# Kernel tuning notes

Hardware: AMD Instinct MI355X
Metric: run time of the kernel (lower is better)

Reference implementation:

```python
import math
import jax, jax.numpy as jnp
import numpy as np

H = 4  # num heads
D = 512
MLP = 1024
EPS = 1e-6


def _ln(x, g, b):
    m = x.mean(-1, keepdims=True)
    v = ((x - m) ** 2).mean(-1, keepdims=True)
    return (x - m) / jnp.sqrt(v + EPS) * g + b


def _heads(x):
    B, S, d = x.shape
    return x.reshape(B, S, H, d // H).transpose(0, 2, 1, 3)  # [B,H,S,hd]


def _att(q, k, v, Wo, bo):
    # q,k,v: [B,S,D] already projected
    hd = q.shape[-1] // H
    qh, kh, vh = _heads(q), _heads(k), _heads(v)
    scores = jnp.einsum('bhqd,bhkd->bhqk', qh, kh) / math.sqrt(hd)
    probs = jax.nn.softmax(scores, axis=-1)
    ctx = jnp.einsum('bhqk,bhkd->bhqd', probs, vh)
    B, _, S, _ = ctx.shape
    ctx = ctx.transpose(0, 2, 1, 3).reshape(B, S, H * hd)
    return ctx @ Wo + bo


def setup_inputs() -> dict:
    key = jax.random.key(0)
    ks = jax.random.split(key, 32)
    i = iter(range(32))
    def w(shape, scale=0.02):
        return jax.random.normal(ks[next(i)], shape, dtype=jnp.float32) * scale
    inp = {
        'x1': jax.random.normal(ks[next(i)], (16, 1024, D), dtype=jnp.float32),
        'x2': jax.random.normal(ks[next(i)], (16, 1024, D), dtype=jnp.float32),
        'ln1_g': jnp.ones((D,), jnp.float32), 'ln1_b': jnp.zeros((D,), jnp.float32),
        'ln2_g': jnp.ones((D,), jnp.float32), 'ln2_b': jnp.zeros((D,), jnp.float32),
        'lnf_g': jnp.ones((D,), jnp.float32), 'lnf_b': jnp.zeros((D,), jnp.float32),
    }
    for name in ['q1', 'k1', 'v1', 'q2', 'k2', 'v2', 'q12', 'k12', 'v12', 'o']:
        inp['W' + name] = w((D, D))
        inp['b' + name] = jnp.zeros((D,), jnp.float32)
    inp['W1'] = w((D, MLP)); inp['b1'] = jnp.zeros((MLP,), jnp.float32)
    inp['W2'] = w((MLP, D)); inp['b2'] = jnp.zeros((D,), jnp.float32)
    return inp


def reference(x1, x2, ln1_g, ln1_b, ln2_g, ln2_b, lnf_g, lnf_b,
              Wq1, bq1, Wk1, bk1, Wv1, bv1,
              Wq2, bq2, Wk2, bk2, Wv2, bv2,
              Wq12, bq12, Wk12, bk12, Wv12, bv12,
              Wo, bo, W1, b1, W2, b2):
    identity = x1
    x1n = _ln(x1, ln1_g, ln1_b)
    x2n = _ln(x2, ln2_g, ln2_b)
    # stream-1 self-attention with residual onto normalized input
    src1 = x1n + _att(x1n @ Wq1 + bq1, x1n @ Wk1 + bk1, x1n @ Wv1 + bv1, Wo, bo)
    # stream-2 self-attention
    src2 = x2n + _att(x2n @ Wq2 + bq2, x2n @ Wk2 + bk2, x2n @ Wv2 + bv2, Wo, bo)
    # cross attention: query from src1, key/value from src2
    attn_out = _att(src1 @ Wq12 + bq12, src2 @ Wk12 + bk12, src2 @ Wv12 + bv12, Wo, bo)
    x = attn_out + identity
    h = _ln(x, lnf_g, lnf_b)
    h = jax.nn.gelu(h @ W1 + b1, approximate=False) @ W2 + b2
    return x + h
```

## Files before the change

kernel.cpp:

```cpp
#include <hip/hip_runtime.h>
#include <math.h>


#define SEQ   1024
#define DM    512
#define HDIM  128
#define MTOK  16384
#define MLPD  1024
#define SC2   ((float)(0.08838834764831845 * 1.4426950408889634))

typedef short bf16x8 __attribute__((ext_vector_type(8)));
typedef float f32x4  __attribute__((ext_vector_type(4)));
typedef float f32x16 __attribute__((ext_vector_type(16)));
typedef unsigned short us4 __attribute__((ext_vector_type(4)));

typedef unsigned int u32g __attribute__((address_space(1)));
typedef unsigned int u32l __attribute__((address_space(3)));

static __device__ __forceinline__ unsigned short f2b(float f) {
  union { float f; unsigned u; } v; v.f = f;
  unsigned r = v.u + 0x7FFFu + ((v.u >> 16) & 1u);
  return (unsigned short)(r >> 16);
}
static __device__ __forceinline__ float b2f(unsigned short h) {
  union { unsigned u; float f; } v; v.u = ((unsigned)h) << 16;
  return v.f;
}
static __device__ __forceinline__ unsigned pk2t(float a, float b) {
  union { float f; unsigned u; } va, vb; va.f = a; vb.f = b;
  return __builtin_amdgcn_perm(vb.u, va.u, 0x07060302u);
}
static __device__ __forceinline__ void gl_lds16(const void* g, void* l) {
  __builtin_amdgcn_global_load_lds((u32g*)g, (u32l*)l, 16, 0, 0);
}

struct P12 { const float* p[12]; };
struct P9  { const float* p[9]; };

__global__ __launch_bounds__(256) void prep_kernel(P12 ws, P9 bs,
                                                   unsigned short* __restrict__ WT0,
                                                   unsigned short* __restrict__ W1t,
                                                   unsigned short* __restrict__ W2t,
                                                   float* __restrict__ bcc) {
  int bid = blockIdx.x;
  if (bid >= 3584) {
    int i = (bid - 3584) * 256 + threadIdx.x;
    if (i < 4608) bcc[i] = bs.p[i >> 9][i & 511];
    return;
  }
  __shared__ float t[32][33];
  const float* W; unsigned short* Wt; int K, N, tt;
  if (bid < 2560)      { int wi = bid >> 8; W = ws.p[wi]; Wt = WT0 + (size_t)wi * 262144; K = 512; N = 512; tt = bid & 255; }
  else if (bid < 3072) { W = ws.p[10]; Wt = W1t; K = 512;  N = 1024; tt = bid - 2560; }
  else                 { W = ws.p[11]; Wt = W2t; K = 1024; N = 512;  tt = bid - 3072; }
  int ntiles = N >> 5;
  int bx = tt % ntiles, by = tt / ntiles;
  int n0 = bx * 32, k0 = by * 32;
  int tx = threadIdx.x & 31, ty = threadIdx.x >> 5;
#pragma unroll
  for (int i = 0; i < 32; i += 8)
    t[ty + i][tx] = W[(size_t)(k0 + ty + i) * N + n0 + tx];
  __syncthreads();
#pragma unroll
  for (int i = 0; i < 32; i += 8)
    Wt[(size_t)(n0 + ty + i) * K + k0 + tx] = f2b(t[tx][ty + i]);
}

__global__ __launch_bounds__(256) void ln_kernel(const float* __restrict__ X0,
                                                 const float* __restrict__ X1,
                                                 const float* __restrict__ g0w,
                                                 const float* __restrict__ b0w,
                                                 const float* __restrict__ g1w,
                                                 const float* __restrict__ b1w,
                                                 unsigned short* __restrict__ out0,
                                                 unsigned short* __restrict__ out1) {
  int idx  = blockIdx.x * 4 + (threadIdx.x >> 6);
  int sel  = idx >> 14;
  int row  = idx & 16383;
  const float* X = sel ? X1 : X0;
  const float* gw = sel ? g1w : g0w;
  const float* bw = sel ? b1w : b0w;
  unsigned short* outB = sel ? out1 : out0;
  int lane = threadIdx.x & 63;
  const float4* xr = (const float4*)(X + (size_t)row * DM);
  float4 a = xr[lane];
  float4 c = xr[lane + 64];
  float s  = a.x + a.y + a.z + a.w + c.x + c.y + c.z + c.w;
  float s2 = a.x*a.x + a.y*a.y + a.z*a.z + a.w*a.w
           + c.x*c.x + c.y*c.y + c.z*c.z + c.w*c.w;
#pragma unroll
  for (int off = 1; off < 64; off <<= 1) {
    s  += __shfl_xor(s,  off, 64);
    s2 += __shfl_xor(s2, off, 64);
  }
  float mean = s * (1.0f / 512.0f);
  float var  = s2 * (1.0f / 512.0f) - mean * mean;
  float rstd = rsqrtf(var + 1e-6f);
  const float4* gv = (const float4*)gw;
  const float4* bv = (const float4*)bw;
  float4 g1 = gv[lane], g2 = gv[lane + 64];
  float4 b1 = bv[lane], b2 = bv[lane + 64];
  us4 o1, o2;
  o1.x = f2b((a.x - mean) * rstd * g1.x + b1.x);
  o1.y = f2b((a.y - mean) * rstd * g1.y + b1.y);
  o1.z = f2b((a.z - mean) * rstd * g1.z + b1.z);
  o1.w = f2b((a.w - mean) * rstd * g1.w + b1.w);
  o2.x = f2b((c.x - mean) * rstd * g2.x + b2.x);
  o2.y = f2b((c.y - mean) * rstd * g2.y + b2.y);
  o2.z = f2b((c.z - mean) * rstd * g2.z + b2.z);
  o2.w = f2b((c.w - mean) * rstd * g2.w + b2.w);
  *(us4*)(outB + (size_t)row * DM + lane * 4)        = o1;
  *(us4*)(outB + (size_t)row * DM + (lane + 64) * 4) = o2;
}

template <int RES, bool GELU_ACT, int OMODE>
__global__ __launch_bounds__(256) void gemm_kernel(const unsigned short* __restrict__ A,
                                                   const unsigned short* __restrict__ A1,
                                                   const unsigned short* __restrict__ Bt,
                                                   const float* __restrict__ bias,
                                                   const void* __restrict__ res,
                                                   float* __restrict__ outF,
                                                   unsigned short* __restrict__ outB,
                                                   unsigned short* __restrict__ outV,
                                                   int M, int N, int K) {
  int nT = N >> 7;
  int mT = M >> 7;
  int xcd = blockIdx.x & 7;
  int idx = blockIdx.x >> 3;
  int mPerX = mT >> 3;
  int q = idx / nT;
  int tm = xcd * mPerX + q;
  int tn = idx - q * nT;
  int m0 = tm << 7, n0 = tn << 7;
  int tid = threadIdx.x, lane = tid & 63, w = tid >> 6;
  int m16 = lane & 15, q4 = lane >> 4;
  int wr = (w & 1) << 6, wc = (w >> 1) << 6;
  __shared__ unsigned short Alds[128 * 64];
  __shared__ unsigned short Blds[128 * 64];
  f32x4 acc[4][4] = {};

  const unsigned short* Aeff = A;
  const unsigned short* Bteff = Bt;
  const float* biaseff = bias;
  if (OMODE == 3) {
    int half = tm >> 7;
    Bteff = Bt + (size_t)half * 3 * 262144;
    biaseff = bias + half * 1536;
  }
  if (OMODE == 4) {
    if (tn >= 4) Aeff = A1;
  }

  for (int k0 = 0; k0 < K; k0 += 64) {
    __syncthreads();
#pragma unroll
    for (int it = 0; it < 4; ++it) {
      int wf   = it * 2048 + w * 512;
      int flat = wf + lane * 8;
      int row  = flat >> 6, kk = flat & 63;
      gl_lds16(Aeff  + (size_t)(m0 + row) * K + k0 + kk, Alds + wf);
      gl_lds16(Bteff + (size_t)(n0 + row) * K + k0 + kk, Blds + wf);
    }
    __syncthreads();
#pragma unroll
    for (int kk = 0; kk < 64; kk += 32) {
      bf16x8 af[4], bfr[4];
#pragma unroll
      for (int i = 0; i < 4; ++i)
        af[i] = *(const bf16x8*)(Alds + (wr + i * 16 + m16) * 64 + kk + q4 * 8);
#pragma unroll
      for (int j = 0; j < 4; ++j)
        bfr[j] = *(const bf16x8*)(Blds + (wc + j * 16 + m16) * 64 + kk + q4 * 8);
#pragma unroll
      for (int i = 0; i < 4; ++i)
#pragma unroll
        for (int j = 0; j < 4; ++j)
          acc[i][j] = __builtin_amdgcn_mfma_f32_16x16x32_bf16(af[i], bfr[j], acc[i][j], 0, 0, 0);
    }
  }
  if (OMODE == 3 || OMODE == 4) {
    if (n0 < 1024) {
      int stride = (OMODE == 3) ? 1024 : 512;
      unsigned short* ob = outB;
      int coff = 0;
      if (OMODE == 4 && n0 >= 512) { ob = outB + (size_t)MTOK * 512; coff = 512; }
      float sc = (n0 < 512) ? SC2 : 1.0f;
#pragma unroll
      for (int i = 0; i < 4; ++i) {
#pragma unroll
        for (int r = 0; r < 4; ++r) {
          int row = m0 + wr + i * 16 + q4 * 4 + r;
#pragma unroll
          for (int j = 0; j < 4; ++j) {
            int col = n0 + wc + j * 16 + m16;
            ob[(size_t)row * stride + col - coff] = f2b((acc[i][j][r] + biaseff[col]) * sc);
          }
        }
      }
    } else {
#pragma unroll
      for (int i = 0; i < 4; ++i) {
        int row0 = m0 + wr + i * 16 + q4 * 4;
        int s = row0 & 1023, bl = row0 >> 10;
        s = (s & ~12) | ((s & 4) << 1) | ((s & 8) >> 1);
#pragma unroll
        for (int j = 0; j < 4; ++j) {
          int col = n0 + wc + j * 16 + m16;
          int hh = (col - 1024) >> 7, hd = col & 127;
          float bb = biaseff[col];
          us4 pkv;
          pkv.x = f2b(acc[i][j][0] + bb);
          pkv.y = f2b(acc[i][j][1] + bb);
          pkv.z = f2b(acc[i][j][2] + bb);
          pkv.w = f2b(acc[i][j][3] + bb);
          *(us4*)(outV + (((size_t)(bl * 4 + hh)) * HDIM + hd) * SEQ + s) = pkv;
        }
      }
    }
  } else {
#pragma unroll
    for (int i = 0; i < 4; ++i) {
#pragma unroll
      for (int r = 0; r < 4; ++r) {
        int row = m0 + wr + i * 16 + q4 * 4 + r;
#pragma unroll
        for (int j = 0; j < 4; ++j) {
          int col = n0 + wc + j * 16 + m16;
          float v = acc[i][j][r] + bias[col];
          if (RES == 1) v += ((const float*)res)[(size_t)row * N + col];
          if (RES == 2) v += b2f(((const unsigned short*)res)[(size_t)row * N + col]);
          if (GELU_ACT) v = 0.5f * v * (1.0f + erff(v * 0.70710678118654752f));
          if (OMODE == 1) outF[(size_t)row * N + col] = v;
          else            outB[(size_t)row * N + col] = f2b(v);
        }
      }
    }
  }
}

__global__ __launch_bounds__(256, 2) void attn_kernel(const unsigned short* __restrict__ Qb_,
                                                      const unsigned short* __restrict__ Kb_,
                                                      int tstride,
                                                      const unsigned short* __restrict__ Vt,
                                                      unsigned short* __restrict__ CTX,
                                                      int pairs_per_xcd) {
  int xcd = blockIdx.x & 7;
  int i   = blockIdx.x >> 3;
  int pair = xcd * pairs_per_xcd + (i >> 3);
  int qt   = i & 7;
  int b = pair >> 2, h = pair & 3;
  int tid = threadIdx.x, lane = tid & 63, w = tid >> 6;
  int m32 = lane & 31, hf = lane >> 5;
  size_t qkoff = ((size_t)b * SEQ) * tstride + h * HDIM;
  const unsigned short* Qg = Qb_ + qkoff;
  const unsigned short* Kg = Kb_ + qkoff;
  const unsigned short* Vp = Vt + (size_t)pair * HDIM * SEQ;

  __shared__ unsigned short Klds[2][64 * 128];
  __shared__ unsigned short Vlds[2][128 * 64];

  int qrow0 = qt * 128 + w * 32;
  bf16x8 qf[8];
  {
    const unsigned short* qp = Qg + (size_t)(qrow0 + m32) * tstride + hf * 8;
#pragma unroll
    for (int ks = 0; ks < 8; ++ks) qf[ks] = *(const bf16x8*)(qp + ks * 16);
  }
  bf16x8 onesf;
#pragma unroll
  for (int j = 0; j < 8; ++j) onesf[j] = (short)0x3F80;

  const unsigned short* kp0 = Kg + (size_t)(16 * w + (lane >> 4)) * tstride
                              + (((lane & 15) ^ (lane >> 4)) << 3);
  const unsigned short* kp1 = Kg + (size_t)(16 * w + 4 + (lane >> 4)) * tstride
                              + (((lane & 15) ^ ((lane >> 4) + 4)) << 3);
  const unsigned short* vp0 = Vp + (size_t)(32 * w + (lane >> 3)) * SEQ
                              + (((lane & 7) ^ (lane >> 3)) << 3);
  int klo = 16 * w * 128;
  int vlo = 32 * w * 64;

  gl_lds16(kp0,               Klds[0] + klo);
  gl_lds16(kp1,               Klds[0] + klo + 4 * 128);
  gl_lds16(kp0 + 8 * tstride, Klds[0] + klo + 8 * 128);
  gl_lds16(kp1 + 8 * tstride, Klds[0] + klo + 12 * 128);
  gl_lds16(vp0,               Vlds[0] + vlo);
  gl_lds16(vp0 + 8 * SEQ,     Vlds[0] + vlo + 8 * 64);
  gl_lds16(vp0 + 16 * SEQ,    Vlds[0] + vlo + 16 * 64);
  gl_lds16(vp0 + 24 * SEQ,    Vlds[0] + vlo + 24 * 64);

  f32x16 o0 = {}, o1 = {}, o2 = {}, o3 = {};
  f32x16 lacc = {};

  for (int kt = 0; kt < 16; ++kt) {
    int cur = kt & 1, nxt = cur ^ 1;
    __syncthreads();
    if (kt < 15) {
      kp0 += 64 * tstride; kp1 += 64 * tstride; vp0 += 64;
      gl_lds16(kp0,               Klds[nxt] + klo);
      gl_lds16(kp1,               Klds[nxt] + klo + 4 * 128);
      gl_lds16(kp0 + 8 * tstride, Klds[nxt] + klo + 8 * 128);
      gl_lds16(kp1 + 8 * tstride, Klds[nxt] + klo + 12 * 128);
      gl_lds16(vp0,               Vlds[nxt] + vlo);
      gl_lds16(vp0 + 8 * SEQ,     Vlds[nxt] + vlo + 8 * 64);
      gl_lds16(vp0 + 16 * SEQ,    Vlds[nxt] + vlo + 16 * 64);
      gl_lds16(vp0 + 24 * SEQ,    Vlds[nxt] + vlo + 24 * 64);
    }
    const unsigned short* Kr = Klds[cur];
    const unsigned short* Vr = Vlds[cur];

    f32x16 sc0 = {}, sc1 = {};
#pragma unroll
    for (int ks = 0; ks < 8; ++ks) {
      int ch = 2 * ks + hf;
      bf16x8 kf0 = *(const bf16x8*)(Kr + m32 * 128 + ((ch ^ (m32 & 7)) << 3));
      sc0 = __builtin_amdgcn_mfma_f32_32x32x16_bf16(kf0, qf[ks], sc0, 0, 0, 0);
      int k1r = 32 + m32;
      bf16x8 kf1 = *(const bf16x8*)(Kr + k1r * 128 + ((ch ^ (k1r & 7)) << 3));
      sc1 = __builtin_amdgcn_mfma_f32_32x32x16_bf16(kf1, qf[ks], sc1, 0, 0, 0);
    }

    bf16x8 pa[4];
#pragma unroll
    for (int t = 0; t < 2; ++t) {
      const f32x16& sc = t ? sc1 : sc0;
#pragma unroll
      for (int g = 0; g < 2; ++g) {
        union { unsigned u[4]; bf16x8 v; } uu;
        uu.u[0] = pk2t(exp2f(sc[8*g+0]), exp2f(sc[8*g+1]));
        uu.u[1] = pk2t(exp2f(sc[8*g+2]), exp2f(sc[8*g+3]));
        uu.u[2] = pk2t(exp2f(sc[8*g+4]), exp2f(sc[8*g+5]));
        uu.u[3] = pk2t(exp2f(sc[8*g+6]), exp2f(sc[8*g+7]));
        pa[2*t + g] = uu.v;
      }
    }

#pragma unroll
    for (int ks = 0; ks < 4; ++ks) {
      int ch = 2 * ks + hf;
      int sw = m32 & 7;
      lacc = __builtin_amdgcn_mfma_f32_32x32x16_bf16(pa[ks], onesf, lacc, 0, 0, 0);
      {
        bf16x8 vf = *(const bf16x8*)(Vr + m32 * 64 + ((ch ^ sw) << 3));
        o0 = __builtin_amdgcn_mfma_f32_32x32x16_bf16(pa[ks], vf, o0, 0, 0, 0);
      }
      {
        bf16x8 vf = *(const bf16x8*)(Vr + (32 + m32) * 64 + ((ch ^ sw) << 3));
        o1 = __builtin_amdgcn_mfma_f32_32x32x16_bf16(pa[ks], vf, o1, 0, 0, 0);
      }
      {
        bf16x8 vf = *(const bf16x8*)(Vr + (64 + m32) * 64 + ((ch ^ sw) << 3));
        o2 = __builtin_amdgcn_mfma_f32_32x32x16_bf16(pa[ks], vf, o2, 0, 0, 0);
      }
      {
        bf16x8 vf = *(const bf16x8*)(Vr + (96 + m32) * 64 + ((ch ^ sw) << 3));
        o3 = __builtin_amdgcn_mfma_f32_32x32x16_bf16(pa[ks], vf, o3, 0, 0, 0);
      }
    }
  }

  size_t obase = ((size_t)b * SEQ + qrow0) * DM + h * HDIM;
#pragma unroll
  for (int g = 0; g < 4; ++g) {
#pragma unroll
    for (int r = 0; r < 4; ++r) {
      int reg = 4 * g + r;
      int rowl = 8 * g + 4 * hf + r;
      float inv = 1.0f / lacc[reg];
      size_t off = obase + (size_t)rowl * DM + m32;
      CTX[off]      = f2b(o0[reg] * inv);
      CTX[off + 32] = f2b(o1[reg] * inv);
      CTX[off + 64] = f2b(o2[reg] * inv);
      CTX[off + 96] = f2b(o3[reg] * inv);
    }
  }
}

extern "C" void kernel_launch(void* const* d_in, const int* in_sizes, int n_in,
                              void* d_out, int out_size, void* d_ws, size_t ws_size,
                              hipStream_t stream) {
  const float* x1    = (const float*)d_in[0];
  const float* x2    = (const float*)d_in[1];
  const float* ln1_g = (const float*)d_in[2];
  const float* ln1_b = (const float*)d_in[3];
  const float* ln2_g = (const float*)d_in[4];
  const float* ln2_b = (const float*)d_in[5];
  const float* lnf_g = (const float*)d_in[6];
  const float* lnf_b = (const float*)d_in[7];
  P12 wsrc;
  for (int i = 0; i < 10; ++i) wsrc.p[i] = (const float*)d_in[8 + 2 * i];
  wsrc.p[10] = (const float*)d_in[28];
  wsrc.p[11] = (const float*)d_in[30];
  P9 bsrc;
  for (int i = 0; i < 9; ++i) bsrc.p[i] = (const float*)d_in[9 + 2 * i];
  const float* bo   = (const float*)d_in[27];
  const float* b1   = (const float*)d_in[29];
  const float* b2   = (const float*)d_in[31];

  char* ws = (char*)d_ws;
  size_t off = 0;
  auto alloc = [&](size_t bytes) -> char* {
    char* p = ws + off;
    off += (bytes + 255) & ~(size_t)255;
    return p;
  };
  unsigned short* WT0 = (unsigned short*)alloc((size_t)10 * 512 * 512 * 2);
  auto WT = [&](int i) { return WT0 + (size_t)i * 262144; };
  unsigned short* W1t = (unsigned short*)alloc((size_t)1024 * 512 * 2);
  unsigned short* W2t = (unsigned short*)alloc((size_t)512 * 1024 * 2);
  float*          bcc = (float*)alloc(4608 * 4);
  unsigned short* XN  = (unsigned short*)alloc((size_t)2 * MTOK * DM * 2);
  unsigned short* QKb = (unsigned short*)alloc((size_t)2 * MTOK * 1024 * 2);
  unsigned short* Vtb = (unsigned short*)alloc((size_t)128 * HDIM * SEQ * 2);
  unsigned short* CT  = (unsigned short*)alloc((size_t)2 * MTOK * DM * 2);
  float*          Xf  = (float*)alloc((size_t)MTOK * DM * 4);
  unsigned short* XN1 = XN + (size_t)MTOK * DM;
  unsigned short* MID = QKb;
  unsigned short* HN  = Vtb;
  float* bias_self  = bcc;
  float* bias_cross = bcc + 3072;

  prep_kernel<<<3602, 256, 0, stream>>>(wsrc, bsrc, WT0, W1t, W2t, bcc);

  ln_kernel<<<2 * MTOK / 4, 256, 0, stream>>>(x1, x2, ln1_g, ln1_b, ln2_g, ln2_b, XN, XN1);

  gemm_kernel<0, false, 3><<<3072, 256, 0, stream>>>(XN, nullptr, WT0, bias_self,
      nullptr, nullptr, QKb, Vtb, 32768, 1536, 512);

  attn_kernel<<<128 * 8, 256, 0, stream>>>(QKb, QKb + 512, 1024, Vtb, CT, 16);

  gemm_kernel<2, false, 0><<<1024, 256, 0, stream>>>(CT, nullptr, WT(9), bo, XN,
      nullptr, XN, nullptr, 32768, 512, 512);

  gemm_kernel<0, false, 4><<<1536, 256, 0, stream>>>(XN, XN1, WT(6), bias_cross,
      nullptr, nullptr, QKb, Vtb, 16384, 1536, 512);

  attn_kernel<<<64 * 8, 256, 0, stream>>>(QKb, QKb + (size_t)MTOK * 512, 512, Vtb, CT, 8);

  gemm_kernel<1, false, 1><<<512, 256, 0, stream>>>(CT, nullptr, WT(9), bo, x1,
      Xf, nullptr, nullptr, 16384, 512, 512);

  ln_kernel<<<MTOK / 4, 256, 0, stream>>>(Xf, Xf, lnf_g, lnf_b, lnf_g, lnf_b, HN, HN);

  gemm_kernel<0, true,  0><<<1024, 256, 0, stream>>>(HN, nullptr, W1t, b1,
      nullptr, nullptr, MID, nullptr, 16384, 1024, 512);
  gemm_kernel<1, false, 1><<<512, 256, 0, stream>>>(MID, nullptr, W2t, b2,
      Xf, (float*)d_out, nullptr, nullptr, 16384, 512, 1024);
}
```

Baseline: 604.2 us.

## Double-buffer GEMM LDS tiles with XOR swizzle and two-block occupancy hint

The GEMM kernel now keeps two LDS buffers for the A and B tiles. It issues the global-to-LDS loads for the next K-step before running the MFMAs on the current one, and drops one barrier per iteration. Tile chunks are stored with an XOR swizzle keyed on the row, so the bf16x8 fragment reads spread across LDS banks. A launch_bounds minimum of two blocks per CU is added. The cost is twice the LDS per block, and register pressure may rise under the occupancy constraint.

```diff
diff --git a/kernel.cpp b/kernel.cpp
--- a/kernel.cpp
+++ b/kernel.cpp
@@ -114,15 +114,15 @@
 }
 
 template <int RES, bool GELU_ACT, int OMODE>
-__global__ __launch_bounds__(256) void gemm_kernel(const unsigned short* __restrict__ A,
-                                                   const unsigned short* __restrict__ A1,
-                                                   const unsigned short* __restrict__ Bt,
-                                                   const float* __restrict__ bias,
-                                                   const void* __restrict__ res,
-                                                   float* __restrict__ outF,
-                                                   unsigned short* __restrict__ outB,
-                                                   unsigned short* __restrict__ outV,
-                                                   int M, int N, int K) {
+__global__ __launch_bounds__(256, 2) void gemm_kernel(const unsigned short* __restrict__ A,
+                                                      const unsigned short* __restrict__ A1,
+                                                      const unsigned short* __restrict__ Bt,
+                                                      const float* __restrict__ bias,
+                                                      const void* __restrict__ res,
+                                                      float* __restrict__ outF,
+                                                      unsigned short* __restrict__ outB,
+                                                      unsigned short* __restrict__ outV,
+                                                      int M, int N, int K) {
   int nT = N >> 7;
   int mT = M >> 7;
   int xcd = blockIdx.x & 7;
@@ -135,8 +135,8 @@
   int tid = threadIdx.x, lane = tid & 63, w = tid >> 6;
   int m16 = lane & 15, q4 = lane >> 4;
   int wr = (w & 1) << 6, wc = (w >> 1) << 6;
-  __shared__ unsigned short Alds[128 * 64];
-  __shared__ unsigned short Blds[128 * 64];
+  __shared__ unsigned short Alds[2][128 * 64];
+  __shared__ unsigned short Blds[2][128 * 64];
   f32x4 acc[4][4] = {};
 
   const unsigned short* Aeff = A;
@@ -151,26 +151,45 @@
     if (tn >= 4) Aeff = A1;
   }
 
-  for (int k0 = 0; k0 < K; k0 += 64) {
+  int srow = lane >> 3;
+  int scol = ((lane & 7) ^ srow) << 3;
+  const unsigned short* Ag = Aeff  + (size_t)(m0 + w * 8 + srow) * K + scol;
+  const unsigned short* Bg = Bteff + (size_t)(n0 + w * 8 + srow) * K + scol;
+  int ldst = w * 512;
+
+#pragma unroll
+  for (int it = 0; it < 4; ++it) {
+    gl_lds16(Ag + (size_t)it * 32 * K, Alds[0] + it * 2048 + ldst);
+    gl_lds16(Bg + (size_t)it * 32 * K, Blds[0] + it * 2048 + ldst);
+  }
+
+  int nk = K >> 6;
+  for (int ks = 0; ks < nk; ++ks) {
+    int cur = ks & 1, nxt = cur ^ 1;
     __syncthreads();
-#pragma unroll
-    for (int it = 0; it < 4; ++it) {
-      int wf   = it * 2048 + w * 512;
-      int flat = wf + lane * 8;
-      int row  = flat >> 6, kk = flat & 63;
-      gl_lds16(Aeff  + (size_t)(m0 + row) * K + k0 + kk, Alds + wf);
-      gl_lds16(Bteff + (size_t)(n0 + row) * K + k0 + kk, Blds + wf);
-    }
-    __syncthreads();
+    if (ks + 1 < nk) {
+      int k0n = (ks + 1) << 6;
+#pragma unroll
+      for (int it = 0; it < 4; ++it) {
+        gl_lds16(Ag + (size_t)it * 32 * K + k0n, Alds[nxt] + it * 2048 + ldst);
+        gl_lds16(Bg + (size_t)it * 32 * K + k0n, Blds[nxt] + it * 2048 + ldst);
+      }
+    }
+    const unsigned short* Ar = Alds[cur];
+    const unsigned short* Br = Blds[cur];
 #pragma unroll
     for (int kk = 0; kk < 64; kk += 32) {
       bf16x8 af[4], bfr[4];
 #pragma unroll
-      for (int i = 0; i < 4; ++i)
-        af[i] = *(const bf16x8*)(Alds + (wr + i * 16 + m16) * 64 + kk + q4 * 8);
-#pragma unroll
-      for (int j = 0; j < 4; ++j)
-        bfr[j] = *(const bf16x8*)(Blds + (wc + j * 16 + m16) * 64 + kk + q4 * 8);
+      for (int i = 0; i < 4; ++i) {
+        int row = wr + i * 16 + m16;
+        af[i] = *(const bf16x8*)(Ar + row * 64 + ((((kk >> 3) + q4) ^ (m16 & 7)) << 3));
+      }
+#pragma unroll
+      for (int j = 0; j < 4; ++j) {
+        int row = wc + j * 16 + m16;
+        bfr[j] = *(const bf16x8*)(Br + row * 64 + ((((kk >> 3) + q4) ^ (m16 & 7)) << 3));
+      }
 #pragma unroll
       for (int i = 0; i < 4; ++i)
 #pragma unroll
```

New measurement: 520.0 us. -13.9%, faster.

## Double-buffer GEMM LDS with swizzled K=32 tiles and raise attention MFMA priority

Applied to the files above, without the earlier changes.

The GEMM main loop now stages K in chunks of 32 through two LDS buffers and prefetches the next chunk while computing the current one, replacing the old load-sync-compute pattern with a single barrier per step. LDS columns are XOR-swizzled to reduce bank conflicts, and launch bounds request 4 blocks per SM. The attention kernel wraps its MFMA sections in s_setprio to favour matrix issue over other waves. This trades more loop iterations and barriers at the smaller K step for overlap of global loads with compute.

```diff
diff --git a/kernel.cpp b/kernel.cpp
--- a/kernel.cpp
+++ b/kernel.cpp
@@ -114,15 +114,15 @@
 }
 
 template <int RES, bool GELU_ACT, int OMODE>
-__global__ __launch_bounds__(256) void gemm_kernel(const unsigned short* __restrict__ A,
-                                                   const unsigned short* __restrict__ A1,
-                                                   const unsigned short* __restrict__ Bt,
-                                                   const float* __restrict__ bias,
-                                                   const void* __restrict__ res,
-                                                   float* __restrict__ outF,
-                                                   unsigned short* __restrict__ outB,
-                                                   unsigned short* __restrict__ outV,
-                                                   int M, int N, int K) {
+__global__ __launch_bounds__(256, 4) void gemm_kernel(const unsigned short* __restrict__ A,
+                                                      const unsigned short* __restrict__ A1,
+                                                      const unsigned short* __restrict__ Bt,
+                                                      const float* __restrict__ bias,
+                                                      const void* __restrict__ res,
+                                                      float* __restrict__ outF,
+                                                      unsigned short* __restrict__ outB,
+                                                      unsigned short* __restrict__ outV,
+                                                      int M, int N, int K) {
   int nT = N >> 7;
   int mT = M >> 7;
   int xcd = blockIdx.x & 7;
@@ -135,8 +135,8 @@
   int tid = threadIdx.x, lane = tid & 63, w = tid >> 6;
   int m16 = lane & 15, q4 = lane >> 4;
   int wr = (w & 1) << 6, wc = (w >> 1) << 6;
-  __shared__ unsigned short Alds[128 * 64];
-  __shared__ unsigned short Blds[128 * 64];
+  __shared__ unsigned short Alds[2][128 * 32];
+  __shared__ unsigned short Blds[2][128 * 32];
   f32x4 acc[4][4] = {};
 
   const unsigned short* Aeff = A;
@@ -151,32 +151,47 @@
     if (tn >= 4) Aeff = A1;
   }
 
-  for (int k0 = 0; k0 < K; k0 += 64) {
+  int swz  = ((lane >> 2) ^ (lane >> 4)) & 3;
+  int scol = ((lane & 3) ^ swz) << 3;
+  const unsigned short* Ag = Aeff  + (size_t)(m0 + w * 16 + (lane >> 2)) * K + scol;
+  const unsigned short* Bg = Bteff + (size_t)(n0 + w * 16 + (lane >> 2)) * K + scol;
+  int ldst = w * 512;
+
+#pragma unroll
+  for (int it = 0; it < 2; ++it) {
+    gl_lds16(Ag + (size_t)it * 64 * K, Alds[0] + it * 2048 + ldst);
+    gl_lds16(Bg + (size_t)it * 64 * K, Blds[0] + it * 2048 + ldst);
+  }
+
+  int rsw  = (m16 ^ (m16 >> 2)) & 3;
+  int roff = (q4 ^ rsw) << 3;
+
+  int nk = K >> 5;
+  for (int ks = 0; ks < nk; ++ks) {
+    int cur = ks & 1, nxt = cur ^ 1;
     __syncthreads();
-#pragma unroll
-    for (int it = 0; it < 4; ++it) {
-      int wf   = it * 2048 + w * 512;
-      int flat = wf + lane * 8;
-      int row  = flat >> 6, kk = flat & 63;
-      gl_lds16(Aeff  + (size_t)(m0 + row) * K + k0 + kk, Alds + wf);
-      gl_lds16(Bteff + (size_t)(n0 + row) * K + k0 + kk, Blds + wf);
-    }
-    __syncthreads();
-#pragma unroll
-    for (int kk = 0; kk < 64; kk += 32) {
-      bf16x8 af[4], bfr[4];
-#pragma unroll
-      for (int i = 0; i < 4; ++i)
-        af[i] = *(const bf16x8*)(Alds + (wr + i * 16 + m16) * 64 + kk + q4 * 8);
+    if (ks + 1 < nk) {
+      int k0n = (ks + 1) << 5;
+#pragma unroll
+      for (int it = 0; it < 2; ++it) {
+        gl_lds16(Ag + (size_t)it * 64 * K + k0n, Alds[nxt] + it * 2048 + ldst);
+        gl_lds16(Bg + (size_t)it * 64 * K + k0n, Blds[nxt] + it * 2048 + ldst);
+      }
+    }
+    const unsigned short* Ar = Alds[cur];
+    const unsigned short* Br = Blds[cur];
+    bf16x8 af[4], bfr[4];
+#pragma unroll
+    for (int i = 0; i < 4; ++i)
+      af[i] = *(const bf16x8*)(Ar + (wr + i * 16 + m16) * 32 + roff);
+#pragma unroll
+    for (int j = 0; j < 4; ++j)
+      bfr[j] = *(const bf16x8*)(Br + (wc + j * 16 + m16) * 32 + roff);
+#pragma unroll
+    for (int i = 0; i < 4; ++i)
 #pragma unroll
       for (int j = 0; j < 4; ++j)
-        bfr[j] = *(const bf16x8*)(Blds + (wc + j * 16 + m16) * 64 + kk + q4 * 8);
-#pragma unroll
-      for (int i = 0; i < 4; ++i)
-#pragma unroll
-        for (int j = 0; j < 4; ++j)
-          acc[i][j] = __builtin_amdgcn_mfma_f32_16x16x32_bf16(af[i], bfr[j], acc[i][j], 0, 0, 0);
-    }
+        acc[i][j] = __builtin_amdgcn_mfma_f32_16x16x32_bf16(af[i], bfr[j], acc[i][j], 0, 0, 0);
   }
   if (OMODE == 3 || OMODE == 4) {
     if (n0 < 1024) {
@@ -308,6 +323,7 @@
     const unsigned short* Kr = Klds[cur];
     const unsigned short* Vr = Vlds[cur];
 
+    __builtin_amdgcn_s_setprio(1);
     f32x16 sc0 = {}, sc1 = {};
 #pragma unroll
     for (int ks = 0; ks < 8; ++ks) {
@@ -318,6 +334,7 @@
       bf16x8 kf1 = *(const bf16x8*)(Kr + k1r * 128 + ((ch ^ (k1r & 7)) << 3));
       sc1 = __builtin_amdgcn_mfma_f32_32x32x16_bf16(kf1, qf[ks], sc1, 0, 0, 0);
     }
+    __builtin_amdgcn_s_setprio(0);
 
     bf16x8 pa[4];
 #pragma unroll
@@ -334,6 +351,7 @@
       }
     }
 
+    __builtin_amdgcn_s_setprio(1);
 #pragma unroll
     for (int ks = 0; ks < 4; ++ks) {
       int ch = 2 * ks + hf;
@@ -356,6 +374,7 @@
         o3 = __builtin_amdgcn_mfma_f32_32x32x16_bf16(pa[ks], vf, o3, 0, 0, 0);
       }
     }
+    __builtin_amdgcn_s_setprio(0);
   }
 
   size_t obase = ((size_t)b * SEQ + qrow0) * DM + h * HDIM;
```

After: 535.7 us. -11.3%, faster.
